# Kernel optimization log

Measured on AMD Instinct MI355X. Metric: run time of the kernel, lower is better.

## Reference

```python
import jax, jax.numpy as jnp
import numpy as np

H = 128  # GRU hidden size

def gru_cell(x, h, Wih, Whh, bih, bhh):
    # torch GRU gate order: r, z, n
    gx = x @ Wih.T + bih          # (B, 3H)
    gh = h @ Whh.T + bhh          # (B, 3H)
    xr, xz, xn = jnp.split(gx, 3, axis=-1)
    hr, hz, hn = jnp.split(gh, 3, axis=-1)
    r = jax.nn.sigmoid(xr + hr)
    z = jax.nn.sigmoid(xz + hz)
    n = jnp.tanh(xn + r * hn)
    return (1.0 - z) * n + z * h

def conv2d(x, w, b, stride):
    y = jax.lax.conv_general_dilated(x, w, window_strides=(stride, stride), padding='VALID',
                                     dimension_numbers=('NCHW', 'OIHW', 'NCHW'))
    return y + b[None, :, None, None]

def setup_inputs() -> dict:
    key = jax.random.key(0)
    ks = jax.random.split(key, 20)
    B, T = 8192, 64
    s = lambda *sh: 0.1
    inp = {
        'cnn_states': jax.random.normal(ks[0], (B, 8, 8, 27), jnp.float32),
        'linears_states': jax.random.normal(ks[1], (B, T, 29), jnp.float32),
        'conv1_w': jax.random.normal(ks[2], (16, 27, 3, 3), jnp.float32) * 0.1,
        'conv1_b': jnp.zeros((16,), jnp.float32),
        'conv2_w': jax.random.normal(ks[3], (32, 16, 2, 2), jnp.float32) * 0.1,
        'conv2_b': jnp.zeros((32,), jnp.float32),
        'fc_w': jax.random.normal(ks[4], (128, 128), jnp.float32) * 0.1,
        'fc_b': jnp.zeros((128,), jnp.float32),
        'enc_Wih': jax.random.normal(ks[5], (3 * H, 29), jnp.float32) * 0.1,
        'enc_Whh': jax.random.normal(ks[6], (3 * H, H), jnp.float32) * 0.1,
        'enc_bih': jnp.zeros((3 * H,), jnp.float32),
        'enc_bhh': jnp.zeros((3 * H,), jnp.float32),
        'dec_Wih': jax.random.normal(ks[7], (3 * H, H), jnp.float32) * 0.1,
        'dec_Whh': jax.random.normal(ks[8], (3 * H, H), jnp.float32) * 0.1,
        'dec_bih': jnp.zeros((3 * H,), jnp.float32),
        'dec_bhh': jnp.zeros((3 * H,), jnp.float32),
        'dis_w': jax.random.normal(ks[9], (78, 256), jnp.float32) * 0.01,
        'dis_b': jnp.zeros((78,), jnp.float32),
        'value_w': jax.random.normal(ks[10], (1, 256), jnp.float32) * 0.1,
        'value_b': jnp.zeros((1,), jnp.float32),
    }
    return inp

def _forward(cnn_states, linears_states, conv1_w, conv1_b, conv2_w, conv2_b, fc_w, fc_b,
             enc_Wih, enc_Whh, enc_bih, enc_bhh, dec_Wih, dec_Whh, dec_bih, dec_bhh,
             dis_w, dis_b, value_w, value_b):
    B, T = linears_states.shape[0], linears_states.shape[1]
    # CNN encoder (NHWC -> NCHW)
    x = jnp.transpose(cnn_states, (0, 3, 1, 2))
    x = jax.nn.relu(conv2d(x, conv1_w, conv1_b, 2))   # (B,16,3,3)
    x = jax.nn.relu(conv2d(x, conv2_w, conv2_b, 1))   # (B,32,2,2)
    x = x.reshape(B, -1)                               # (B,128), CHW order matches torch Flatten
    z_cnn = jax.nn.relu(x @ fc_w.T + fc_b)             # (B,128)

    # encoder GRU over linears_states
    xs = jnp.transpose(linears_states, (1, 0, 2))      # (T,B,29)
    h0 = jnp.zeros((B, H), linears_states.dtype)
    def enc_step(h, xt):
        h2 = gru_cell(xt, h, enc_Wih, enc_Whh, enc_bih, enc_bhh)
        return h2, None
    h_enc, _ = jax.lax.scan(enc_step, h0, xs)

    x0 = jnp.zeros((B, H), linears_states.dtype)
    def dec_step(carry, _):
        xin, h = carry
        h2 = gru_cell(xin, h, dec_Wih, dec_Whh, dec_bih, dec_bhh)
        return (h2, h2), None
    (z_pn, _), _ = jax.lax.scan(dec_step, (x0, h_enc), None, length=T)

    pn = jnp.concatenate([z_cnn, z_pn], axis=1)        # (B,256)
    distris = pn @ dis_w.T + dis_b                     # (B,78)
    value = pn @ value_w.T + value_b                   # (B,1)
    return distris, value

def reference(cnn_states, linears_states, conv1_w, conv1_b, conv2_w, conv2_b, fc_w, fc_b,
              enc_Wih, enc_Whh, enc_bih, enc_bhh, dec_Wih, dec_Whh, dec_bih, dec_bhh,
              dis_w, dis_b, value_w, value_b):
    return _forward(cnn_states, linears_states, conv1_w, conv1_b, conv2_w, conv2_b, fc_w, fc_b,
                    enc_Wih, enc_Whh, enc_bih, enc_bhh, dec_Wih, dec_Whh, dec_bih, dec_bhh,
                    dis_w, dis_b, value_w, value_b)
```

## Files before the change

### kernel.cpp

```cpp
#include <hip/hip_runtime.h>

typedef _Float16 f16;
typedef _Float16 f16x8 __attribute__((ext_vector_type(8)));
typedef float f32x4 __attribute__((ext_vector_type(4)));

#define WS_EWIH 4194304
#define WS_EWHH 4218880
#define WS_DWC  4317184
#define WS_DWHH 4448256
#define WS_BIAS 4546560
#define WS_W1F  4550656
#define WS_W2F  4559872
#define WS_FCWF 4563968

static __device__ __forceinline__ f32x4 mfma16(f16x8 a, f16x8 b, f32x4 c) {
    return __builtin_amdgcn_mfma_f32_16x16x32_f16(a, b, c, 0, 0, 0);
}
static __device__ __forceinline__ float fexp2n(float x) {
    return __builtin_amdgcn_exp2f(x * -1.4426950408889634f);
}

__global__ void k_prep(const float* __restrict__ eWih, const float* __restrict__ eWhh,
                       const float* __restrict__ ebih, const float* __restrict__ ebhh,
                       const float* __restrict__ dWih, const float* __restrict__ dWhh,
                       const float* __restrict__ dbih, const float* __restrict__ dbhh,
                       const float* __restrict__ w1, const float* __restrict__ w2,
                       const float* __restrict__ fcw,
                       char* __restrict__ ws)
{
    f16* ewih = (f16*)(ws + WS_EWIH);
    f16* ewhh = (f16*)(ws + WS_EWHH);
    f16* dwc  = (f16*)(ws + WS_DWC);
    f16* dwhh = (f16*)(ws + WS_DWHH);
    float* bias = (float*)(ws + WS_BIAS);
    f16* w1f = (f16*)(ws + WS_W1F);
    f16* w2f = (f16*)(ws + WS_W2F);
    f16* fcwf = (f16*)(ws + WS_FCWF);
    const int total = 12288 + 49152 + 65536 + 49152 + 1024 + 4608 + 2048 + 16384;
    for (int i = blockIdx.x * 256 + threadIdx.x; i < total; i += gridDim.x * 256) {
        int j = i;
        if (j < 12288) { int g = j >> 5, k = j & 31;
            ewih[j] = (f16)((k < 29) ? eWih[g * 29 + k] : 0.0f); continue; }
        j -= 12288;
        if (j < 49152) { ewhh[j] = (f16)eWhh[j]; continue; }
        j -= 49152;
        if (j < 65536) { int row = j >> 7, k = j & 127; float v;
            if (row < 256)      v = dWih[row * 128 + k] + dWhh[row * 128 + k];
            else if (row < 384) v = dWih[row * 128 + k];
            else                v = dWhh[(row - 128) * 128 + k];
            dwc[j] = (f16)v; continue; }
        j -= 65536;
        if (j < 49152) { dwhh[j] = (f16)dWhh[j]; continue; }
        j -= 49152;
        if (j < 1024) {
            if (j < 256)        bias[j] = ebih[j] + ebhh[j];
            else if (j < 384)   bias[j] = ebih[j];
            else if (j < 512)   bias[j] = ebhh[j - 128];
            else if (j < 768)   bias[j] = dbih[j - 512] + dbhh[j - 512];
            else if (j < 896)   bias[j] = dbih[j - 512];
            else                bias[j] = dbhh[j - 640];
            continue; }
        j -= 1024;
        if (j < 4608) {
            int kk = j >> 9, rem = j & 511, co = rem >> 5, k = rem & 31;
            w1f[j] = (f16)((k < 27) ? w1[co * 243 + k * 9 + kk] : 0.0f); continue; }
        j -= 4608;
        if (j < 2048) {
            int s = j >> 10, rem = j & 1023, co = rem >> 5, k = rem & 31;
            int kk2 = 2 * s + (k >= 16), ci = k & 15;
            w2f[j] = (f16)w2[co * 64 + ci * 4 + kk2]; continue; }
        j -= 2048;
        fcwf[j] = (f16)fcw[j];
    }
}

__global__ __launch_bounds__(512, 4) void k_gru(
    const float* __restrict__ cin,
    const float* __restrict__ lin,
    const float* __restrict__ b1, const float* __restrict__ b2,
    const float* __restrict__ fcb,
    const char* __restrict__ ws,
    const float* __restrict__ dis_w, const float* __restrict__ dis_b,
    const float* __restrict__ value_w, const float* __restrict__ value_b,
    float* __restrict__ out)
{
    __shared__ __align__(16) char smem[32000];
    f16 (*h_s)[16][136]  = (f16(*)[16][136])(smem);
    f16 (*x_s)[16][32]   = (f16(*)[16][32])(smem + 8704);
    float (*pn_s)[264]   = (float(*)[264])(smem + 10752);
    f16 (*a1f)[9][24]    = (f16(*)[9][24])(smem);
    f16 (*vf)[136]       = (f16(*)[136])(smem + 27648);

    const int tid = threadIdx.x;
    const int wv = tid >> 6;
    const int lane = tid & 63;
    const int nl = lane & 15;
    const int quad = lane >> 4;
    const int j0 = wv * 16;
    const int row0 = blockIdx.x * 16;

    const f16* ewih = (const f16*)(ws + WS_EWIH);
    const f16* ewhh = (const f16*)(ws + WS_EWHH);
    const f16* dwc  = (const f16*)(ws + WS_DWC);
    const f16* dwhh = (const f16*)(ws + WS_DWHH);
    const float* bias = (const float*)(ws + WS_BIAS);
    const f16* w1f = (const f16*)(ws + WS_W1F);
    const f16* w2f = (const f16*)(ws + WS_W2F);
    const f16* fcwf = (const f16*)(ws + WS_FCWF);

    {
        const float* imgp = cin + (size_t)(row0 + nl) * 1728 + quad * 8;
        float b1v = b1[nl];
        for (int p = wv; p < 9; p += 8) {
            int oy = p / 3, ox = p % 3;
            f32x4 acc = {b1v, b1v, b1v, b1v};
            #pragma unroll
            for (int kk = 0; kk < 9; kk++) {
                f16x8 bw = *(const f16x8*)(w1f + (kk * 16 + nl) * 32 + quad * 8);
                int pix = (2 * oy + kk / 3) * 8 + (2 * ox + kk % 3);
                const float* s = imgp + pix * 27;
                f16x8 a;
                #pragma unroll
                for (int jj = 0; jj < 8; jj++) a[jj] = (f16)s[jj];
                acc = mfma16(a, bw, acc);
            }
            #pragma unroll
            for (int r = 0; r < 4; r++)
                a1f[quad * 4 + r][p][nl] = (f16)fmaxf(acc[r], 0.0f);
        }
        __syncthreads();
        {
            int pos = wv >> 1, nt = wv & 1;
            int y = pos >> 1, x = pos & 1;
            float bv = b2[nt * 16 + nl];
            f32x4 acc = {bv, bv, bv, bv};
            #pragma unroll
            for (int s = 0; s < 2; s++) {
                int kk2 = 2 * s + (quad >> 1);
                int pos1 = (y + (kk2 >> 1)) * 3 + (x + (kk2 & 1));
                f16x8 a = *(const f16x8*)(&a1f[nl][pos1][(quad & 1) * 8]);
                f16x8 b = *(const f16x8*)(w2f + ((size_t)s * 32 + nt * 16 + nl) * 32 + quad * 8);
                acc = mfma16(a, b, acc);
            }
            #pragma unroll
            for (int r = 0; r < 4; r++)
                vf[quad * 4 + r][(nt * 16 + nl) * 4 + (y * 2 + x)] = (f16)fmaxf(acc[r], 0.0f);
        }
        __syncthreads();
        {
            int o = wv * 16 + nl;
            float bv = fcb[o];
            f32x4 acc = {bv, bv, bv, bv};
            #pragma unroll
            for (int kt = 0; kt < 4; kt++) {
                f16x8 a = *(const f16x8*)(&vf[nl][kt * 32 + quad * 8]);
                f16x8 b = *(const f16x8*)(fcwf + o * 128 + kt * 32 + quad * 8);
                acc = mfma16(a, b, acc);
            }
            #pragma unroll
            for (int r = 0; r < 4; r++)
                pn_s[quad * 4 + r][o] = fmaxf(acc[r], 0.0f);
        }
        __syncthreads();
    }

    for (int i = tid; i < 2 * 16 * 136; i += 512) ((f16*)h_s)[i] = (f16)0.0f;

    const int rsw = (nl & 8) ? 16 : 0;
    const int wrow = quad * 4;
    const int wsw = (quad >= 2) ? 16 : 0;
    const int wcol = (j0 + nl + wsw) & 127;
    const int c0 = (quad * 8 + rsw) & 127;
    const int c1 = (32 + quad * 8 + rsw) & 127;
    const int c2 = (64 + quad * 8 + rsw) & 127;
    const int c3 = (96 + quad * 8 + rsw) & 127;

    float ho[4];
    #pragma unroll
    for (int r = 0; r < 4; r++) ho[r] = 0.0f;

    const int xr = tid >> 5, xc = tid & 31;
    const bool xok = (xc < 29);
    const size_t lin_base = (size_t)(row0 + xr) * 1856 + xc;

    {
        float eb_r, eb_z, eb_xn, eb_hn;
        { int c = j0 + nl;
          eb_r = bias[c]; eb_z = bias[128 + c]; eb_xn = bias[256 + c]; eb_hn = bias[384 + c]; }
        f16x8 we_r[4], we_z[4], we_hn[4], we_xr, we_xz, we_xn;
        { int gr = j0 + nl;
          #pragma unroll
          for (int kt = 0; kt < 4; kt++) {
              we_r[kt]  = *(const f16x8*)(ewhh + gr * 128 + kt * 32 + quad * 8);
              we_z[kt]  = *(const f16x8*)(ewhh + (128 + gr) * 128 + kt * 32 + quad * 8);
              we_hn[kt] = *(const f16x8*)(ewhh + (256 + gr) * 128 + kt * 32 + quad * 8);
          }
          we_xr = *(const f16x8*)(ewih + gr * 32 + quad * 8);
          we_xz = *(const f16x8*)(ewih + (128 + gr) * 32 + quad * 8);
          we_xn = *(const f16x8*)(ewih + (256 + gr) * 32 + quad * 8);
        }

        float xv = xok ? lin[lin_base] : 0.0f;

#define ENC_STEP(BUF, OBUF, TN)                                                      \
        do {                                                                         \
            x_s[BUF][xr][xc] = (f16)xv;                                              \
            __syncthreads();                                                         \
            f16x8 ax = *(const f16x8*)(&x_s[BUF][nl][quad * 8]);                     \
            f16x8 ah0 = *(const f16x8*)(&h_s[BUF][nl][c0]);                          \
            f16x8 ah1 = *(const f16x8*)(&h_s[BUF][nl][c1]);                          \
            f16x8 ah2 = *(const f16x8*)(&h_s[BUF][nl][c2]);                          \
            f16x8 ah3 = *(const f16x8*)(&h_s[BUF][nl][c3]);                          \
            if ((TN) < 64) xv = xok ? lin[lin_base + (TN) * 29] : 0.0f;              \
            f32x4 aR  = {eb_r, eb_r, eb_r, eb_r};                                    \
            f32x4 aZ  = {eb_z, eb_z, eb_z, eb_z};                                    \
            f32x4 aXN = {eb_xn, eb_xn, eb_xn, eb_xn};                                \
            f32x4 aHN = {eb_hn, eb_hn, eb_hn, eb_hn};                                \
            aR  = mfma16(ax, we_xr, aR);                                             \
            aZ  = mfma16(ax, we_xz, aZ);                                             \
            aXN = mfma16(ax, we_xn, aXN);                                            \
            aR  = mfma16(ah0, we_r[0], aR);  aR  = mfma16(ah1, we_r[1], aR);         \
            aR  = mfma16(ah2, we_r[2], aR);  aR  = mfma16(ah3, we_r[3], aR);         \
            aZ  = mfma16(ah0, we_z[0], aZ);  aZ  = mfma16(ah1, we_z[1], aZ);         \
            aZ  = mfma16(ah2, we_z[2], aZ);  aZ  = mfma16(ah3, we_z[3], aZ);         \
            aHN = mfma16(ah0, we_hn[0], aHN); aHN = mfma16(ah1, we_hn[1], aHN);      \
            aHN = mfma16(ah2, we_hn[2], aHN); aHN = mfma16(ah3, we_hn[3], aHN);      \
            _Pragma("unroll")                                                        \
            for (int r = 0; r < 4; r++) {                                            \
                float ea = fexp2n(aR[r]), eb = fexp2n(aZ[r]);                        \
                float s1 = 1.0f + ea, s2 = 1.0f + eb;                                \
                float R = __builtin_amdgcn_rcpf(s1 * s2);                            \
                float rg = s2 * R, zg = s1 * R;                                      \
                float ec = fexp2n(2.0f * (aXN[r] + rg * aHN[r]));                    \
                float ng = (1.0f - ec) * __builtin_amdgcn_rcpf(1.0f + ec);           \
                float h = ng + zg * (ho[r] - ng);                                    \
                ho[r] = h;                                                           \
                h_s[OBUF][wrow + r][wcol] = (f16)h;                                  \
            }                                                                        \
        } while (0)

        for (int t = 0; t < 64; t += 2) {
            ENC_STEP(0, 1, t + 1);
            ENC_STEP(1, 0, t + 2);
        }
#undef ENC_STEP
    }

    float db_r, db_z, db_xn, db_hn;
    { int c = j0 + nl;
      db_r = bias[512 + c]; db_z = bias[640 + c]; db_xn = bias[768 + c]; db_hn = bias[896 + c]; }

    {
        __syncthreads();
        f16x8 ah0 = *(const f16x8*)(&h_s[0][nl][c0]);
        f16x8 ah1 = *(const f16x8*)(&h_s[0][nl][c1]);
        f16x8 ah2 = *(const f16x8*)(&h_s[0][nl][c2]);
        f16x8 ah3 = *(const f16x8*)(&h_s[0][nl][c3]);
        int gr = j0 + nl;
        f32x4 aR  = {db_r, db_r, db_r, db_r};
        f32x4 aZ  = {db_z, db_z, db_z, db_z};
        f32x4 aHN = {db_hn, db_hn, db_hn, db_hn};
        #pragma unroll
        for (int kt = 0; kt < 4; kt++) {
            f16x8 b0 = *(const f16x8*)(dwhh + gr * 128 + kt * 32 + quad * 8);
            f16x8 b1 = *(const f16x8*)(dwhh + (128 + gr) * 128 + kt * 32 + quad * 8);
            f16x8 b2 = *(const f16x8*)(dwhh + (256 + gr) * 128 + kt * 32 + quad * 8);
            f16x8 a = (kt == 0) ? ah0 : (kt == 1) ? ah1 : (kt == 2) ? ah2 : ah3;
            aR  = mfma16(a, b0, aR);
            aZ  = mfma16(a, b1, aZ);
            aHN = mfma16(a, b2, aHN);
        }
        #pragma unroll
        for (int r = 0; r < 4; r++) {
            float ea = fexp2n(aR[r]), eb = fexp2n(aZ[r]);
            float s1 = 1.0f + ea, s2 = 1.0f + eb;
            float R = __builtin_amdgcn_rcpf(s1 * s2);
            float rg = s2 * R, zg = s1 * R;
            float ec = fexp2n(2.0f * (db_xn + rg * aHN[r]));
            float ng = (1.0f - ec) * __builtin_amdgcn_rcpf(1.0f + ec);
            float h = ng + zg * (ho[r] - ng);
            ho[r] = h;
            h_s[1][wrow + r][wcol] = (f16)h;
        }
    }
    {
        f16x8 wd_r[4], wd_z[4], wd_xn[4], wd_hn[4];
        { int gr = j0 + nl;
          #pragma unroll
          for (int kt = 0; kt < 4; kt++) {
              wd_r[kt]  = *(const f16x8*)(dwc + gr * 128 + kt * 32 + quad * 8);
              wd_z[kt]  = *(const f16x8*)(dwc + (128 + gr) * 128 + kt * 32 + quad * 8);
              wd_xn[kt] = *(const f16x8*)(dwc + (256 + gr) * 128 + kt * 32 + quad * 8);
              wd_hn[kt] = *(const f16x8*)(dwc + (384 + gr) * 128 + kt * 32 + quad * 8);
          }
        }

#define DEC_STEP(BUF, OBUF)                                                          \
        do {                                                                         \
            __syncthreads();                                                         \
            f16x8 ah0 = *(const f16x8*)(&h_s[BUF][nl][c0]);                          \
            f16x8 ah1 = *(const f16x8*)(&h_s[BUF][nl][c1]);                          \
            f16x8 ah2 = *(const f16x8*)(&h_s[BUF][nl][c2]);                          \
            f16x8 ah3 = *(const f16x8*)(&h_s[BUF][nl][c3]);                          \
            f32x4 aR  = {db_r, db_r, db_r, db_r};                                    \
            f32x4 aZ  = {db_z, db_z, db_z, db_z};                                    \
            f32x4 aXN = {db_xn, db_xn, db_xn, db_xn};                                \
            f32x4 aHN = {db_hn, db_hn, db_hn, db_hn};                                \
            aR  = mfma16(ah0, wd_r[0], aR);   aR  = mfma16(ah1, wd_r[1], aR);        \
            aR  = mfma16(ah2, wd_r[2], aR);   aR  = mfma16(ah3, wd_r[3], aR);        \
            aZ  = mfma16(ah0, wd_z[0], aZ);   aZ  = mfma16(ah1, wd_z[1], aZ);        \
            aZ  = mfma16(ah2, wd_z[2], aZ);   aZ  = mfma16(ah3, wd_z[3], aZ);        \
            aXN = mfma16(ah0, wd_xn[0], aXN); aXN = mfma16(ah1, wd_xn[1], aXN);      \
            aXN = mfma16(ah2, wd_xn[2], aXN); aXN = mfma16(ah3, wd_xn[3], aXN);      \
            aHN = mfma16(ah0, wd_hn[0], aHN); aHN = mfma16(ah1, wd_hn[1], aHN);      \
            aHN = mfma16(ah2, wd_hn[2], aHN); aHN = mfma16(ah3, wd_hn[3], aHN);      \
            _Pragma("unroll")                                                        \
            for (int r = 0; r < 4; r++) {                                            \
                float ea = fexp2n(aR[r]), eb = fexp2n(aZ[r]);                        \
                float s1 = 1.0f + ea, s2 = 1.0f + eb;                                \
                float R = __builtin_amdgcn_rcpf(s1 * s2);                            \
                float rg = s2 * R, zg = s1 * R;                                      \
                float ec = fexp2n(2.0f * (aXN[r] + rg * aHN[r]));                    \
                float ng = (1.0f - ec) * __builtin_amdgcn_rcpf(1.0f + ec);           \
                float h = ng + zg * (ho[r] - ng);                                    \
                ho[r] = h;                                                           \
                h_s[OBUF][wrow + r][wcol] = (f16)h;                                  \
            }                                                                        \
        } while (0)

        DEC_STEP(1, 0);
        for (int t = 2; t < 64; t += 2) {
            DEC_STEP(0, 1);
            DEC_STEP(1, 0);
        }
#undef DEC_STEP
    }

    #pragma unroll
    for (int r = 0; r < 4; r++)
        pn_s[wrow + r][128 + j0 + nl] = ho[r];
    __syncthreads();

    const int rr = tid & 15, og = tid >> 4;
    const float4* pr4 = (const float4*)(&pn_s[rr][0]);
    for (int o = og; o < 79; o += 32) {
        const float* wrow_p = (o < 78) ? (dis_w + o * 256) : value_w;
        float acc = (o < 78) ? dis_b[o] : value_b[0];
        const float4* wr4 = (const float4*)wrow_p;
        #pragma unroll 8
        for (int k = 0; k < 64; k++) {
            float4 a = wr4[k], b = pr4[k];
            acc += a.x * b.x + a.y * b.y + a.z * b.z + a.w * b.w;
        }
        if (o < 78) out[(size_t)(row0 + rr) * 78 + o] = acc;
        else        out[(size_t)8192 * 78 + row0 + rr] = acc;
    }
}

extern "C" void kernel_launch(void* const* d_in, const int* in_sizes, int n_in,
                              void* d_out, int out_size, void* d_ws, size_t ws_size,
                              hipStream_t stream)
{
    (void)in_sizes; (void)n_in; (void)out_size; (void)ws_size;
    const float* cnn  = (const float*)d_in[0];
    const float* lin  = (const float*)d_in[1];
    const float* c1w  = (const float*)d_in[2];
    const float* c1b  = (const float*)d_in[3];
    const float* c2w  = (const float*)d_in[4];
    const float* c2b  = (const float*)d_in[5];
    const float* fcw  = (const float*)d_in[6];
    const float* fcb  = (const float*)d_in[7];
    const float* eWih = (const float*)d_in[8];
    const float* eWhh = (const float*)d_in[9];
    const float* ebih = (const float*)d_in[10];
    const float* ebhh = (const float*)d_in[11];
    const float* dWih = (const float*)d_in[12];
    const float* dWhh = (const float*)d_in[13];
    const float* dbih = (const float*)d_in[14];
    const float* dbhh = (const float*)d_in[15];
    const float* disw = (const float*)d_in[16];
    const float* disb = (const float*)d_in[17];
    const float* vw   = (const float*)d_in[18];
    const float* vb   = (const float*)d_in[19];
    char* ws = (char*)d_ws;
    float* out = (float*)d_out;

    hipLaunchKernelGGL(k_prep, dim3(128), dim3(256), 0, stream,
                       eWih, eWhh, ebih, ebhh, dWih, dWhh, dbih, dbhh,
                       c1w, c2w, fcw, ws);
    hipLaunchKernelGGL(k_gru, dim3(512), dim3(512), 0, stream,
                       cnn, lin, c1b, c2b, fcb, ws, disw, disb, vw, vb, out);
}
```

Before: 331.3 us.

## Process two 16-row batch tiles per block to interleave independent GRU chains

Each block now handles 32 batch rows as two independent 16-row tiles, with the grid halved to 256 blocks. Every MFMA and gate computation is duplicated for tiles A and B, sharing the register-resident weights and one barrier per timestep. The goal is to hide MFMA and transcendental latency with two independent dependency chains and to halve the number of barriers per row. In exchange, register and LDS pressure roughly double (launch bounds drop to 2 blocks), and only 256 blocks are left, which may underfill the 256 CUs.

Measured after the change: 348.1 us. 1.05x slower.

```diff
diff --git a/kernel.cpp b/kernel.cpp
--- a/kernel.cpp
+++ b/kernel.cpp
@@ -74,7 +74,7 @@
     }
 }
 
-__global__ __launch_bounds__(512, 4) void k_gru(
+__global__ __launch_bounds__(512, 2) void k_gru(
     const float* __restrict__ cin,
     const float* __restrict__ lin,
     const float* __restrict__ b1, const float* __restrict__ b2,
@@ -84,12 +84,12 @@
     const float* __restrict__ value_w, const float* __restrict__ value_b,
     float* __restrict__ out)
 {
-    __shared__ __align__(16) char smem[32000];
-    f16 (*h_s)[16][136]  = (f16(*)[16][136])(smem);
-    f16 (*x_s)[16][32]   = (f16(*)[16][32])(smem + 8704);
-    float (*pn_s)[264]   = (float(*)[264])(smem + 10752);
-    f16 (*a1f)[9][24]    = (f16(*)[9][24])(smem);
-    f16 (*vf)[136]       = (f16(*)[136])(smem + 27648);
+    __shared__ __align__(16) char smem[55296];
+    f16 (*h_s)[2][16][136]  = (f16(*)[2][16][136])(smem);
+    f16 (*x_s)[2][16][32]   = (f16(*)[2][16][32])(smem + 17408);
+    float (*pn_s)[264]      = (float(*)[264])(smem + 21504);
+    f16 (*a1f)[9][24]       = (f16(*)[9][24])(smem);
+    f16 (*vf)[136]          = (f16(*)[136])(smem + 8704);
 
     const int tid = threadIdx.x;
     const int wv = tid >> 6;
@@ -97,7 +97,7 @@
     const int nl = lane & 15;
     const int quad = lane >> 4;
     const int j0 = wv * 16;
-    const int row0 = blockIdx.x * 16;
+    const int row0 = blockIdx.x * 32;
 
     const f16* ewih = (const f16*)(ws + WS_EWIH);
     const f16* ewhh = (const f16*)(ws + WS_EWHH);
@@ -108,8 +108,8 @@
     const f16* w2f = (const f16*)(ws + WS_W2F);
     const f16* fcwf = (const f16*)(ws + WS_FCWF);
 
-    {
-        const float* imgp = cin + (size_t)(row0 + nl) * 1728 + quad * 8;
+    for (int g = 0; g < 2; g++) {
+        const float* imgp = cin + (size_t)(row0 + g * 16 + nl) * 1728 + quad * 8;
         float b1v = b1[nl];
         for (int p = wv; p < 9; p += 8) {
             int oy = p / 3, ox = p % 3;
@@ -159,12 +159,12 @@
             }
             #pragma unroll
             for (int r = 0; r < 4; r++)
-                pn_s[quad * 4 + r][o] = fmaxf(acc[r], 0.0f);
+                pn_s[g * 16 + quad * 4 + r][o] = fmaxf(acc[r], 0.0f);
         }
         __syncthreads();
     }
 
-    for (int i = tid; i < 2 * 16 * 136; i += 512) ((f16*)h_s)[i] = (f16)0.0f;
+    for (int i = tid; i < 2 * 2 * 16 * 136; i += 512) ((f16*)h_s)[i] = (f16)0.0f;
 
     const int rsw = (nl & 8) ? 16 : 0;
     const int wrow = quad * 4;
@@ -175,13 +175,28 @@
     const int c2 = (64 + quad * 8 + rsw) & 127;
     const int c3 = (96 + quad * 8 + rsw) & 127;
 
-    float ho[4];
+    float hoA[4], hoB[4];
     #pragma unroll
-    for (int r = 0; r < 4; r++) ho[r] = 0.0f;
+    for (int r = 0; r < 4; r++) { hoA[r] = 0.0f; hoB[r] = 0.0f; }
 
     const int xr = tid >> 5, xc = tid & 31;
     const bool xok = (xc < 29);
-    const size_t lin_base = (size_t)(row0 + xr) * 1856 + xc;
+    const size_t lin_baseA = (size_t)(row0 + xr) * 1856 + xc;
+    const size_t lin_baseB = (size_t)(row0 + 16 + xr) * 1856 + xc;
+
+#define GATES(AR, AZ, AXN, AHN, HO, OB, TI, BR, BZ, BXN, BHN)                        \
+        _Pragma("unroll")                                                            \
+        for (int r = 0; r < 4; r++) {                                                \
+            float ea = fexp2n((AR)[r]), eb = fexp2n((AZ)[r]);                        \
+            float s1 = 1.0f + ea, s2 = 1.0f + eb;                                    \
+            float R = __builtin_amdgcn_rcpf(s1 * s2);                                \
+            float rg = s2 * R, zg = s1 * R;                                          \
+            float ec = fexp2n(2.0f * ((AXN)[r] + rg * (AHN)[r]));                    \
+            float ng = (1.0f - ec) * __builtin_amdgcn_rcpf(1.0f + ec);               \
+            float h = ng + zg * ((HO)[r] - ng);                                      \
+            (HO)[r] = h;                                                             \
+            h_s[OB][TI][wrow + r][wcol] = (f16)h;                                    \
+        }
 
     {
         float eb_r, eb_z, eb_xn, eb_hn;
@@ -200,43 +215,49 @@
           we_xn = *(const f16x8*)(ewih + (256 + gr) * 32 + quad * 8);
         }
 
-        float xv = xok ? lin[lin_base] : 0.0f;
+        float xvA = xok ? lin[lin_baseA] : 0.0f;
+        float xvB = xok ? lin[lin_baseB] : 0.0f;
 
 #define ENC_STEP(BUF, OBUF, TN)                                                      \
         do {                                                                         \
-            x_s[BUF][xr][xc] = (f16)xv;                                              \
+            x_s[BUF][0][xr][xc] = (f16)xvA;                                          \
+            x_s[BUF][1][xr][xc] = (f16)xvB;                                          \
             __syncthreads();                                                         \
-            f16x8 ax = *(const f16x8*)(&x_s[BUF][nl][quad * 8]);                     \
-            f16x8 ah0 = *(const f16x8*)(&h_s[BUF][nl][c0]);                          \
-            f16x8 ah1 = *(const f16x8*)(&h_s[BUF][nl][c1]);                          \
-            f16x8 ah2 = *(const f16x8*)(&h_s[BUF][nl][c2]);                          \
-            f16x8 ah3 = *(const f16x8*)(&h_s[BUF][nl][c3]);                          \
-            if ((TN) < 64) xv = xok ? lin[lin_base + (TN) * 29] : 0.0f;              \
-            f32x4 aR  = {eb_r, eb_r, eb_r, eb_r};                                    \
-            f32x4 aZ  = {eb_z, eb_z, eb_z, eb_z};                                    \
-            f32x4 aXN = {eb_xn, eb_xn, eb_xn, eb_xn};                                \
-            f32x4 aHN = {eb_hn, eb_hn, eb_hn, eb_hn};                                \
-            aR  = mfma16(ax, we_xr, aR);                                             \
-            aZ  = mfma16(ax, we_xz, aZ);                                             \
-            aXN = mfma16(ax, we_xn, aXN);                                            \
-            aR  = mfma16(ah0, we_r[0], aR);  aR  = mfma16(ah1, we_r[1], aR);         \
-            aR  = mfma16(ah2, we_r[2], aR);  aR  = mfma16(ah3, we_r[3], aR);         \
-            aZ  = mfma16(ah0, we_z[0], aZ);  aZ  = mfma16(ah1, we_z[1], aZ);         \
-            aZ  = mfma16(ah2, we_z[2], aZ);  aZ  = mfma16(ah3, we_z[3], aZ);         \
-            aHN = mfma16(ah0, we_hn[0], aHN); aHN = mfma16(ah1, we_hn[1], aHN);      \
-            aHN = mfma16(ah2, we_hn[2], aHN); aHN = mfma16(ah3, we_hn[3], aHN);      \
-            _Pragma("unroll")                                                        \
-            for (int r = 0; r < 4; r++) {                                            \
-                float ea = fexp2n(aR[r]), eb = fexp2n(aZ[r]);                        \
-                float s1 = 1.0f + ea, s2 = 1.0f + eb;                                \
-                float R = __builtin_amdgcn_rcpf(s1 * s2);                            \
-                float rg = s2 * R, zg = s1 * R;                                      \
-                float ec = fexp2n(2.0f * (aXN[r] + rg * aHN[r]));                    \
-                float ng = (1.0f - ec) * __builtin_amdgcn_rcpf(1.0f + ec);           \
-                float h = ng + zg * (ho[r] - ng);                                    \
-                ho[r] = h;                                                           \
-                h_s[OBUF][wrow + r][wcol] = (f16)h;                                  \
+            f16x8 axA = *(const f16x8*)(&x_s[BUF][0][nl][quad * 8]);                 \
+            f16x8 axB = *(const f16x8*)(&x_s[BUF][1][nl][quad * 8]);                 \
+            f16x8 aA0 = *(const f16x8*)(&h_s[BUF][0][nl][c0]);                       \
+            f16x8 aA1 = *(const f16x8*)(&h_s[BUF][0][nl][c1]);                       \
+            f16x8 aA2 = *(const f16x8*)(&h_s[BUF][0][nl][c2]);                       \
+            f16x8 aA3 = *(const f16x8*)(&h_s[BUF][0][nl][c3]);                       \
+            f16x8 aB0 = *(const f16x8*)(&h_s[BUF][1][nl][c0]);                       \
+            f16x8 aB1 = *(const f16x8*)(&h_s[BUF][1][nl][c1]);                       \
+            f16x8 aB2 = *(const f16x8*)(&h_s[BUF][1][nl][c2]);                       \
+            f16x8 aB3 = *(const f16x8*)(&h_s[BUF][1][nl][c3]);                       \
+            if ((TN) < 64) {                                                         \
+                xvA = xok ? lin[lin_baseA + (TN) * 29] : 0.0f;                       \
+                xvB = xok ? lin[lin_baseB + (TN) * 29] : 0.0f;                       \
             }                                                                        \
+            f32x4 aRA  = {eb_r, eb_r, eb_r, eb_r},   aRB  = aRA;                     \
+            f32x4 aZA  = {eb_z, eb_z, eb_z, eb_z},   aZB  = aZA;                     \
+            f32x4 aXNA = {eb_xn, eb_xn, eb_xn, eb_xn}, aXNB = aXNA;                  \
+            f32x4 aHNA = {eb_hn, eb_hn, eb_hn, eb_hn}, aHNB = aHNA;                  \
+            aRA  = mfma16(axA, we_xr, aRA);   aRB  = mfma16(axB, we_xr, aRB);        \
+            aZA  = mfma16(axA, we_xz, aZA);   aZB  = mfma16(axB, we_xz, aZB);        \
+            aXNA = mfma16(axA, we_xn, aXNA);  aXNB = mfma16(axB, we_xn, aXNB);       \
+            aRA  = mfma16(aA0, we_r[0], aRA);  aRB  = mfma16(aB0, we_r[0], aRB);     \
+            aRA  = mfma16(aA1, we_r[1], aRA);  aRB  = mfma16(aB1, we_r[1], aRB);     \
+            aRA  = mfma16(aA2, we_r[2], aRA);  aRB  = mfma16(aB2, we_r[2], aRB);     \
+            aRA  = mfma16(aA3, we_r[3], aRA);  aRB  = mfma16(aB3, we_r[3], aRB);     \
+            aZA  = mfma16(aA0, we_z[0], aZA);  aZB  = mfma16(aB0, we_z[0], aZB);     \
+            aZA  = mfma16(aA1, we_z[1], aZA);  aZB  = mfma16(aB1, we_z[1], aZB);     \
+            aZA  = mfma16(aA2, we_z[2], aZA);  aZB  = mfma16(aB2, we_z[2], aZB);     \
+            aZA  = mfma16(aA3, we_z[3], aZA);  aZB  = mfma16(aB3, we_z[3], aZB);     \
+            aHNA = mfma16(aA0, we_hn[0], aHNA); aHNB = mfma16(aB0, we_hn[0], aHNB);  \
+            aHNA = mfma16(aA1, we_hn[1], aHNA); aHNB = mfma16(aB1, we_hn[1], aHNB);  \
+            aHNA = mfma16(aA2, we_hn[2], aHNA); aHNB = mfma16(aB2, we_hn[2], aHNB);  \
+            aHNA = mfma16(aA3, we_hn[3], aHNA); aHNB = mfma16(aB3, we_hn[3], aHNB);  \
+            GATES(aRA, aZA, aXNA, aHNA, hoA, OBUF, 0, , , , )                        \
+            GATES(aRB, aZB, aXNB, aHNB, hoB, OBUF, 1, , , , )                        \
         } while (0)
 
         for (int t = 0; t < 64; t += 2) {
@@ -252,35 +273,52 @@
 
     {
         __syncthreads();
-        f16x8 ah0 = *(const f16x8*)(&h_s[0][nl][c0]);
-        f16x8 ah1 = *(const f16x8*)(&h_s[0][nl][c1]);
-        f16x8 ah2 = *(const f16x8*)(&h_s[0][nl][c2]);
-        f16x8 ah3 = *(const f16x8*)(&h_s[0][nl][c3]);
+        f16x8 aA0 = *(const f16x8*)(&h_s[0][0][nl][c0]);
+        f16x8 aA1 = *(const f16x8*)(&h_s[0][0][nl][c1]);
+        f16x8 aA2 = *(const f16x8*)(&h_s[0][0][nl][c2]);
+        f16x8 aA3 = *(const f16x8*)(&h_s[0][0][nl][c3]);
+        f16x8 aB0 = *(const f16x8*)(&h_s[0][1][nl][c0]);
+        f16x8 aB1 = *(const f16x8*)(&h_s[0][1][nl][c1]);
+        f16x8 aB2 = *(const f16x8*)(&h_s[0][1][nl][c2]);
+        f16x8 aB3 = *(const f16x8*)(&h_s[0][1][nl][c3]);
         int gr = j0 + nl;
-        f32x4 aR  = {db_r, db_r, db_r, db_r};
-        f32x4 aZ  = {db_z, db_z, db_z, db_z};
-        f32x4 aHN = {db_hn, db_hn, db_hn, db_hn};
+        f32x4 aRA  = {db_r, db_r, db_r, db_r},   aRB  = aRA;
+        f32x4 aZA  = {db_z, db_z, db_z, db_z},   aZB  = aZA;
+        f32x4 aHNA = {db_hn, db_hn, db_hn, db_hn}, aHNB = aHNA;
         #pragma unroll
         for (int kt = 0; kt < 4; kt++) {
             f16x8 b0 = *(const f16x8*)(dwhh + gr * 128 + kt * 32 + quad * 8);
             f16x8 b1 = *(const f16x8*)(dwhh + (128 + gr) * 128 + kt * 32 + quad * 8);
             f16x8 b2 = *(const f16x8*)(dwhh + (256 + gr) * 128 + kt * 32 + quad * 8);
-            f16x8 a = (kt == 0) ? ah0 : (kt == 1) ? ah1 : (kt == 2) ? ah2 : ah3;
-            aR  = mfma16(a, b0, aR);
-            aZ  = mfma16(a, b1, aZ);
-            aHN = mfma16(a, b2, aHN);
+            f16x8 aA = (kt == 0) ? aA0 : (kt == 1) ? aA1 : (kt == 2) ? aA2 : aA3;
+            f16x8 aB = (kt == 0) ? aB0 : (kt == 1) ? aB1 : (kt == 2) ? aB2 : aB3;
+            aRA  = mfma16(aA, b0, aRA);   aRB  = mfma16(aB, b0, aRB);
+            aZA  = mfma16(aA, b1, aZA);   aZB  = mfma16(aB, b1, aZB);
+            aHNA = mfma16(aA, b2, aHNA);  aHNB = mfma16(aB, b2, aHNB);
         }
         #pragma unroll
         for (int r = 0; r < 4; r++) {
-            float ea = fexp2n(aR[r]), eb = fexp2n(aZ[r]);
+            float ea = fexp2n(aRA[r]), eb = fexp2n(aZA[r]);
             float s1 = 1.0f + ea, s2 = 1.0f + eb;
             float R = __builtin_amdgcn_rcpf(s1 * s2);
             float rg = s2 * R, zg = s1 * R;
-            float ec = fexp2n(2.0f * (db_xn + rg * aHN[r]));
+            float ec = fexp2n(2.0f * (db_xn + rg * aHNA[r]));
             float ng = (1.0f - ec) * __builtin_amdgcn_rcpf(1.0f + ec);
-            float h = ng + zg * (ho[r] - ng);
-            ho[r] = h;
-            h_s[1][wrow + r][wcol] = (f16)h;
+            float h = ng + zg * (hoA[r] - ng);
+            hoA[r] = h;
+            h_s[1][0][wrow + r][wcol] = (f16)h;
+        }
+        #pragma unroll
+        for (int r = 0; r < 4; r++) {
+            float ea = fexp2n(aRB[r]), eb = fexp2n(aZB[r]);
+            float s1 = 1.0f + ea, s2 = 1.0f + eb;
+            float R = __builtin_amdgcn_rcpf(s1 * s2);
+            float rg = s2 * R, zg = s1 * R;
+            float ec = fexp2n(2.0f * (db_xn + rg * aHNB[r]));
+            float ng = (1.0f - ec) * __builtin_amdgcn_rcpf(1.0f + ec);
+            float h = ng + zg * (hoB[r] - ng);
+            hoB[r] = h;
+            h_s[1][1][wrow + r][wcol] = (f16)h;
         }
     }
     {
@@ -298,34 +336,36 @@
 #define DEC_STEP(BUF, OBUF)                                                          \
         do {                                                                         \
             __syncthreads();                                                         \
-            f16x8 ah0 = *(const f16x8*)(&h_s[BUF][nl][c0]);                          \
-            f16x8 ah1 = *(const f16x8*)(&h_s[BUF][nl][c1]);                          \
-            f16x8 ah2 = *(const f16x8*)(&h_s[BUF][nl][c2]);                          \
-            f16x8 ah3 = *(const f16x8*)(&h_s[BUF][nl][c3]);                          \
-            f32x4 aR  = {db_r, db_r, db_r, db_r};                                    \
-            f32x4 aZ  = {db_z, db_z, db_z, db_z};                                    \
-            f32x4 aXN = {db_xn, db_xn, db_xn, db_xn};                                \
-            f32x4 aHN = {db_hn, db_hn, db_hn, db_hn};                                \
-            aR  = mfma16(ah0, wd_r[0], aR);   aR  = mfma16(ah1, wd_r[1], aR);        \
-            aR  = mfma16(ah2, wd_r[2], aR);   aR  = mfma16(ah3, wd_r[3], aR);        \
-            aZ  = mfma16(ah0, wd_z[0], aZ);   aZ  = mfma16(ah1, wd_z[1], aZ);        \
-            aZ  = mfma16(ah2, wd_z[2], aZ);   aZ  = mfma16(ah3, wd_z[3], aZ);        \
-            aXN = mfma16(ah0, wd_xn[0], aXN); aXN = mfma16(ah1, wd_xn[1], aXN);      \
-            aXN = mfma16(ah2, wd_xn[2], aXN); aXN = mfma16(ah3, wd_xn[3], aXN);      \
-            aHN = mfma16(ah0, wd_hn[0], aHN); aHN = mfma16(ah1, wd_hn[1], aHN);      \
-            aHN = mfma16(ah2, wd_hn[2], aHN); aHN = mfma16(ah3, wd_hn[3], aHN);      \
-            _Pragma("unroll")                                                        \
-            for (int r = 0; r < 4; r++) {                                            \
-                float ea = fexp2n(aR[r]), eb = fexp2n(aZ[r]);                        \
-                float s1 = 1.0f + ea, s2 = 1.0f + eb;                                \
-                float R = __builtin_amdgcn_rcpf(s1 * s2);                            \
-                float rg = s2 * R, zg = s1 * R;                                      \
-                float ec = fexp2n(2.0f * (aXN[r] + rg * aHN[r]));                    \
-                float ng = (1.0f - ec) * __builtin_amdgcn_rcpf(1.0f + ec);           \
-                float h = ng + zg * (ho[r] - ng);                                    \
-                ho[r] = h;                                                           \
-                h_s[OBUF][wrow + r][wcol] = (f16)h;                                  \
-            }                                                                        \
+            f16x8 aA0 = *(const f16x8*)(&h_s[BUF][0][nl][c0]);                       \
+            f16x8 aA1 = *(const f16x8*)(&h_s[BUF][0][nl][c1]);                       \
+            f16x8 aA2 = *(const f16x8*)(&h_s[BUF][0][nl][c2]);                       \
+            f16x8 aA3 = *(const f16x8*)(&h_s[BUF][0][nl][c3]);                       \
+            f16x8 aB0 = *(const f16x8*)(&h_s[BUF][1][nl][c0]);                       \
+            f16x8 aB1 = *(const f16x8*)(&h_s[BUF][1][nl][c1]);                       \
+            f16x8 aB2 = *(const f16x8*)(&h_s[BUF][1][nl][c2]);                       \
+            f16x8 aB3 = *(const f16x8*)(&h_s[BUF][1][nl][c3]);                       \
+            f32x4 aRA  = {db_r, db_r, db_r, db_r},   aRB  = aRA;                     \
+            f32x4 aZA  = {db_z, db_z, db_z, db_z},   aZB  = aZA;                     \
+            f32x4 aXNA = {db_xn, db_xn, db_xn, db_xn}, aXNB = aXNA;                  \
+            f32x4 aHNA = {db_hn, db_hn, db_hn, db_hn}, aHNB = aHNA;                  \
+            aRA  = mfma16(aA0, wd_r[0], aRA);   aRB  = mfma16(aB0, wd_r[0], aRB);    \
+            aRA  = mfma16(aA1, wd_r[1], aRA);   aRB  = mfma16(aB1, wd_r[1], aRB);    \
+            aRA  = mfma16(aA2, wd_r[2], aRA);   aRB  = mfma16(aB2, wd_r[2], aRB);    \
+            aRA  = mfma16(aA3, wd_r[3], aRA);   aRB  = mfma16(aB3, wd_r[3], aRB);    \
+            aZA  = mfma16(aA0, wd_z[0], aZA);   aZB  = mfma16(aB0, wd_z[0], aZB);    \
+            aZA  = mfma16(aA1, wd_z[1], aZA);   aZB  = mfma16(aB1, wd_z[1], aZB);    \
+            aZA  = mfma16(aA2, wd_z[2], aZA);   aZB  = mfma16(aB2, wd_z[2], aZB);    \
+            aZA  = mfma16(aA3, wd_z[3], aZA);   aZB  = mfma16(aB3, wd_z[3], aZB);    \
+            aXNA = mfma16(aA0, wd_xn[0], aXNA); aXNB = mfma16(aB0, wd_xn[0], aXNB);  \
+            aXNA = mfma16(aA1, wd_xn[1], aXNA); aXNB = mfma16(aB1, wd_xn[1], aXNB);  \
+            aXNA = mfma16(aA2, wd_xn[2], aXNA); aXNB = mfma16(aB2, wd_xn[2], aXNB);  \
+            aXNA = mfma16(aA3, wd_xn[3], aXNA); aXNB = mfma16(aB3, wd_xn[3], aXNB);  \
+            aHNA = mfma16(aA0, wd_hn[0], aHNA); aHNB = mfma16(aB0, wd_hn[0], aHNB);  \
+            aHNA = mfma16(aA1, wd_hn[1], aHNA); aHNB = mfma16(aB1, wd_hn[1], aHNB);  \
+            aHNA = mfma16(aA2, wd_hn[2], aHNA); aHNB = mfma16(aB2, wd_hn[2], aHNB);  \
+            aHNA = mfma16(aA3, wd_hn[3], aHNA); aHNB = mfma16(aB3, wd_hn[3], aHNB);  \
+            GATES(aRA, aZA, aXNA, aHNA, hoA, OBUF, 0, , , , )                        \
+            GATES(aRB, aZB, aXNB, aHNB, hoB, OBUF, 1, , , , )                        \
         } while (0)
 
         DEC_STEP(1, 0);
@@ -334,16 +374,19 @@
             DEC_STEP(1, 0);
         }
 #undef DEC_STEP
+#undef GATES
     }
 
     #pragma unroll
-    for (int r = 0; r < 4; r++)
-        pn_s[wrow + r][128 + j0 + nl] = ho[r];
+    for (int r = 0; r < 4; r++) {
+        pn_s[wrow + r][128 + j0 + nl] = hoA[r];
+        pn_s[16 + wrow + r][128 + j0 + nl] = hoB[r];
+    }
     __syncthreads();
 
-    const int rr = tid & 15, og = tid >> 4;
+    const int rr = tid & 31, og = tid >> 5;
     const float4* pr4 = (const float4*)(&pn_s[rr][0]);
-    for (int o = og; o < 79; o += 32) {
+    for (int o = og; o < 79; o += 16) {
         const float* wrow_p = (o < 78) ? (dis_w + o * 256) : value_w;
         float acc = (o < 78) ? dis_b[o] : value_b[0];
         const float4* wr4 = (const float4*)wrow_p;
@@ -388,6 +431,6 @@
     hipLaunchKernelGGL(k_prep, dim3(128), dim3(256), 0, stream,
                        eWih, eWhh, ebih, ebhh, dWih, dWhh, dbih, dbhh,
                        c1w, c2w, fcw, ws);
-    hipLaunchKernelGGL(k_gru, dim3(512), dim3(512), 0, stream,
+    hipLaunchKernelGGL(k_gru, dim3(256), dim3(512), 0, stream,
                        cnn, lin, c1b, c2b, fcb, ws, disw, disb, vw, vb, out);
 }
```
